# Performance work log

Hardware: AMD Instinct MI355X
Metric: run time of the kernel (lower is better)

The kernel has to match this reference:

```python
import jax, jax.numpy as jnp
import numpy as np

K_HEADS = 8
D_HEAD = 64
D = K_HEADS * D_HEAD  # 512
B, TP, TQ, N = 8, 48, 48, 256


def setup_inputs() -> dict:
    key = jax.random.key(0)
    ks = jax.random.split(key, 13)
    s = 1.0 / np.sqrt(D)
    inp = {
        "X": jax.random.normal(ks[0], (B, TP, N, D), jnp.float32),
        "STE_P": jax.random.normal(ks[1], (B, TP, N, D), jnp.float32),
        "STE_Q": jax.random.normal(ks[2], (B, TQ, N, D), jnp.float32),
        "Wq": jax.random.uniform(ks[3], (D, D), jnp.float32, -s, s),
        "bq": jax.random.uniform(ks[4], (D,), jnp.float32, -s, s),
        "Wk": jax.random.uniform(ks[5], (D, D), jnp.float32, -s, s),
        "bk": jax.random.uniform(ks[6], (D,), jnp.float32, -s, s),
        "Wv": jax.random.uniform(ks[7], (D, D), jnp.float32, -s, s),
        "bv": jax.random.uniform(ks[8], (D,), jnp.float32, -s, s),
        "W1": jax.random.uniform(ks[9], (D, D), jnp.float32, -s, s),
        "b1": jax.random.uniform(ks[10], (D,), jnp.float32, -s, s),
        "W2": jax.random.uniform(ks[11], (D, D), jnp.float32, -s, s),
        "b2": jax.random.uniform(ks[12], (D,), jnp.float32, -s, s),
    }
    return inp


def reference(X, STE_P, STE_Q, Wq, bq, Wk, bk, Wv, bv, W1, b1, W2, b2):
    # ReLU-fused QKV projections
    q = jax.nn.relu(STE_Q @ Wq + bq)  # [B, Tq, N, D]
    k = jax.nn.relu(STE_P @ Wk + bk)  # [B, Tp, N, D]
    v = jax.nn.relu(X @ Wv + bv)      # [B, Tp, N, D]

    # split(last, d) + cat(dim 0) == introduce head axis h of size K
    b, tq, n, _ = q.shape
    tp = k.shape[1]
    q = q.reshape(b, tq, n, K_HEADS, D_HEAD)
    k = k.reshape(b, tp, n, K_HEADS, D_HEAD)
    v = v.reshape(b, tp, n, K_HEADS, D_HEAD)

    # attention over the TIME axis, per node and head: scores [b,h,n,tq,tp]
    scale = 1.0 / jnp.sqrt(jnp.asarray(D_HEAD, q.dtype))
    attn = jnp.einsum('bqnhd,bpnhd->bhnqp', q, k) * scale
    attn = jax.nn.softmax(attn, axis=-1)
    out = jnp.einsum('bhnqp,bpnhd->bqnhd', attn, v).reshape(b, tq, n, D)

    out = jax.nn.relu(out @ W1 + b1) @ W2 + b2
    return out
```

## Files before the change

### kernel.cpp

```cpp
#include <hip/hip_runtime.h>

typedef _Float16 f16;
typedef __fp16 hf2 __attribute__((ext_vector_type(2)));
typedef _Float16 f16x4 __attribute__((ext_vector_type(4)));
typedef _Float16 f16x8 __attribute__((ext_vector_type(8)));
typedef float f32x4 __attribute__((ext_vector_type(4)));

typedef const __attribute__((address_space(1))) unsigned int guint;
typedef __attribute__((address_space(3))) unsigned int luint;
__device__ __forceinline__ void gl_lds16(const void* g, void* l) {
    __builtin_amdgcn_global_load_lds((guint*)g, (luint*)l, 16, 0, 0);
}
template <int N>
__device__ __forceinline__ void vmwait() {
    if constexpr (N == 8)       asm volatile("s_waitcnt vmcnt(8)" ::: "memory");
    else if constexpr (N == 6)  asm volatile("s_waitcnt vmcnt(6)" ::: "memory");
    else if constexpr (N == 4)  asm volatile("s_waitcnt vmcnt(4)" ::: "memory");
    else                        asm volatile("s_waitcnt vmcnt(0)" ::: "memory");
}
__device__ __forceinline__ void barrier_raw() { __builtin_amdgcn_s_barrier(); __builtin_amdgcn_sched_barrier(0); }
__device__ __forceinline__ void lgkm0() { asm volatile("s_waitcnt lgkmcnt(0)" ::: "memory"); }

__device__ __forceinline__ f16x8 pack8(float4 x0, float4 x1) {
    hf2 p0 = __builtin_amdgcn_cvt_pkrtz(x0.x, x0.y);
    hf2 p1 = __builtin_amdgcn_cvt_pkrtz(x0.z, x0.w);
    hf2 p2 = __builtin_amdgcn_cvt_pkrtz(x1.x, x1.y);
    hf2 p3 = __builtin_amdgcn_cvt_pkrtz(x1.z, x1.w);
    f16x8 h;
    h[0] = (f16)p0[0]; h[1] = (f16)p0[1]; h[2] = (f16)p1[0]; h[3] = (f16)p1[1];
    h[4] = (f16)p2[0]; h[5] = (f16)p2[1]; h[6] = (f16)p3[0]; h[7] = (f16)p3[1];
    return h;
}

__global__ __launch_bounds__(256) void wconv(const float* w0, const float* w1, const float* w2,
                                             const float* w3, const float* w4, f16* dst) {
    const float* src;
    switch (blockIdx.z) { case 0: src = w0; break; case 1: src = w1; break;
                          case 2: src = w2; break; case 3: src = w3; break; default: src = w4; }
    __shared__ float tile[32][33];
    int k0 = blockIdx.x * 32, n0 = blockIdx.y * 32;
    int t = threadIdx.x;
    int r = t >> 3, c4 = (t & 7) * 4;
    float4 v = *(const float4*)(src + (k0 + r) * 512 + n0 + c4);
    tile[r][c4 + 0] = v.x; tile[r][c4 + 1] = v.y; tile[r][c4 + 2] = v.z; tile[r][c4 + 3] = v.w;
    __syncthreads();
    f16x4 o;
    o[0] = (f16)tile[c4 + 0][r]; o[1] = (f16)tile[c4 + 1][r];
    o[2] = (f16)tile[c4 + 2][r]; o[3] = (f16)tile[c4 + 3][r];
    *(f16x4*)(dst + (size_t)blockIdx.z * 262144 + (n0 + r) * 512 + k0 + c4) = o;
}

__global__ __launch_bounds__(512, 2) void gemm_qkv3(const float* __restrict__ A0, const float* __restrict__ A1,
                                                    const float* __restrict__ A2,
                                                    const f16* __restrict__ B0, const f16* __restrict__ B1,
                                                    const f16* __restrict__ B2,
                                                    const float* __restrict__ bias0, const float* __restrict__ bias1,
                                                    const float* __restrict__ bias2,
                                                    f16* __restrict__ C0, f16* __restrict__ C1,
                                                    f16* __restrict__ C2) {
    constexpr int BUFSZ = 32768;
    __shared__ __align__(16) char smem[4 * BUFSZ];

    const int cpx = gridDim.x >> 3;
    const int orig = blockIdx.x;
    const int wgid = (orig & 7) * cpx + (orig >> 3);
    const int mid = wgid / 768;
    const int sub = wgid - mid * 768;
    const int by = sub & 1, bx = sub >> 1;
    const int r0 = bx * 256, c0 = by * 256;

    const float* A   = (mid == 0) ? A0 : (mid == 1) ? A1 : A2;
    const f16* Bt    = (mid == 0) ? B0 : (mid == 1) ? B1 : B2;
    const float* bias = (mid == 0) ? bias0 : (mid == 1) ? bias1 : bias2;
    f16* Cp          = (mid == 0) ? C0 : (mid == 1) ? C1 : C2;

    const int t = threadIdx.x, j = t & 63, w = t >> 6;
    const int lr = j & 15, lq = j >> 4;
    const int wr = (w >> 2) * 128, wc = (w & 3) * 64;

    const float* aS = A + (size_t)(r0 + (t >> 1)) * 512 + (t & 1) * 16;
    const int awRow = t >> 1;
    const int awS = (t >> 2) & 3;
    const int awc = (t & 1) * 2;
    const int aw0 = awRow * 64 + ((awc ^ awS) << 4);
    const int aw1 = awRow * 64 + (((awc + 1) ^ awS) << 4);

    const int srow = t >> 2;
    const int sblk = (t & 3) ^ ((t >> 3) & 3);
    const f16* bS = Bt + (size_t)(c0 + srow) * 512 + sblk * 8;
    const int dstT = t * 16;

    int aoff[8], boff[4];
#pragma unroll
    for (int m = 0; m < 8; m++) {
        int row = wr + m * 16 + lr;
        aoff[m] = row * 64 + ((lq ^ ((row >> 1) & 3)) << 4);
    }
#pragma unroll
    for (int nb = 0; nb < 4; nb++) {
        int row = wc + nb * 16 + lr;
        boff[nb] = 16384 + row * 64 + ((lq ^ ((row >> 1) & 3)) << 4);
    }

    f32x4 acc[8][4] = {};
    float4 rgA[4], rgB[4];

    auto loadTo = [&](int kt, float4* rg) {
        const float* p = aS + kt * 32;
        rg[0] = *(const float4*)p;
        rg[1] = *(const float4*)(p + 4);
        rg[2] = *(const float4*)(p + 8);
        rg[3] = *(const float4*)(p + 12);
    };
    auto writeA = [&](const float4* rg, int buf) {
        char* base = smem + buf * BUFSZ;
        *(f16x8*)(base + aw0) = pack8(rg[0], rg[1]);
        *(f16x8*)(base + aw1) = pack8(rg[2], rg[3]);
    };
    auto stageB = [&](int kt) {
        char* d = smem + (kt & 3) * BUFSZ + 16384 + dstT;
        const f16* s = bS + kt * 32;
        gl_lds16(s, d);
        gl_lds16(s + 65536, d + 8192);
    };

#define PHASE_A(kt, bfr)                                                    \
    do {                                                                    \
        const char* sb_ = smem + ((kt) & 3) * BUFSZ;                        \
        f16x8 afr[4];                                                       \
        _Pragma("unroll")                                                   \
        for (int nb = 0; nb < 4; nb++) bfr[nb] = *(const f16x8*)(sb_ + boff[nb]); \
        _Pragma("unroll")                                                   \
        for (int m = 0; m < 4; m++) afr[m] = *(const f16x8*)(sb_ + aoff[m]); \
        __builtin_amdgcn_s_setprio(1);                                      \
        _Pragma("unroll")                                                   \
        for (int m = 0; m < 4; m++)                                         \
            _Pragma("unroll")                                               \
            for (int nb = 0; nb < 4; nb++)                                  \
                acc[m][nb] = __builtin_amdgcn_mfma_f32_16x16x32_f16(afr[m], bfr[nb], acc[m][nb], 0, 0, 0); \
        __builtin_amdgcn_s_setprio(0);                                      \
    } while (0)

#define PHASE_B(kt, bfr)                                                    \
    do {                                                                    \
        const char* sb_ = smem + ((kt) & 3) * BUFSZ;                        \
        f16x8 afr2[4];                                                      \
        _Pragma("unroll")                                                   \
        for (int m = 0; m < 4; m++) afr2[m] = *(const f16x8*)(sb_ + aoff[m + 4]); \
        __builtin_amdgcn_s_setprio(1);                                      \
        _Pragma("unroll")                                                   \
        for (int m = 0; m < 4; m++)                                         \
            _Pragma("unroll")                                               \
            for (int nb = 0; nb < 4; nb++)                                  \
                acc[m + 4][nb] = __builtin_amdgcn_mfma_f32_16x16x32_f16(afr2[m], bfr[nb], acc[m + 4][nb], 0, 0, 0); \
        __builtin_amdgcn_s_setprio(0);                                      \
    } while (0)

    loadTo(0, rgA);
    stageB(0); stageB(1);
    loadTo(1, rgB);
    stageB(2);
    vmwait<8>();
    __builtin_amdgcn_sched_barrier(0);
    writeA(rgA, 0);
    lgkm0();
    barrier_raw();

#pragma unroll 1
    for (int k2 = 0; k2 < 8; ++k2) {
        {
            const int kt = 2 * k2;
            if (k2 <= 6) loadTo(kt + 2, rgA);
            if (k2 <= 6) vmwait<6>(); else vmwait<0>();
            __builtin_amdgcn_sched_barrier(0);
            writeA(rgB, (kt + 1) & 3);
            f16x8 bfr[4];
            PHASE_A(kt, bfr);
            barrier_raw();
            if (k2 <= 6) stageB(kt + 3);
            PHASE_B(kt, bfr);
            lgkm0();
            barrier_raw();
        }
        {
            const int kt = 2 * k2 + 1;
            if (k2 <= 6) loadTo(kt + 2, rgB);
            if (k2 <= 6) vmwait<6>(); else vmwait<0>();
            __builtin_amdgcn_sched_barrier(0);
            if (k2 <= 6) writeA(rgA, (kt + 1) & 3);
            f16x8 bfr[4];
            PHASE_A(kt, bfr);
            barrier_raw();
            if (k2 <= 5) stageB(kt + 3);
            PHASE_B(kt, bfr);
            lgkm0();
            barrier_raw();
        }
    }
#undef PHASE_A
#undef PHASE_B

#pragma unroll
    for (int nb = 0; nb < 4; nb++) {
        int col = wc + nb * 16 + lr;
        float b = bias[c0 + col];
#pragma unroll
        for (int m = 0; m < 8; m++) {
#pragma unroll
            for (int r = 0; r < 4; r++) {
                float v = fmaxf(acc[m][nb][r] + b, 0.0f);
                int row = wr + m * 16 + lq * 4 + r;
                int pblk = (col >> 3) ^ (row & 31);
                *(f16*)(smem + row * 512 + (pblk << 4) + (col & 7) * 2) = (f16)v;
            }
        }
    }
    lgkm0();
    barrier_raw();
#pragma unroll
    for (int i = 0; i < 16; i++) {
        int ci = i * 512 + t;
        int row = ci >> 5, blk = ci & 31;
        int pblk = blk ^ (row & 31);
        f16x8 vle = *(const f16x8*)(smem + row * 512 + (pblk << 4));
        *(f16x8*)(Cp + (size_t)(r0 + row) * 512 + c0 + blk * 8) = vle;
    }
}

template <bool RELU, bool O16>
__global__ __launch_bounds__(512, 2) void gemm_8ph(const f16* __restrict__ A,
                                                   const f16* __restrict__ Bt,
                                                   const float* __restrict__ bias,
                                                   void* __restrict__ Cp) {
    constexpr int BUFSZ = 32768;
    __shared__ __align__(16) char smem[4 * BUFSZ];

    const int cpx = gridDim.x >> 3;
    const int orig = blockIdx.x;
    const int wgid = (orig & 7) * cpx + (orig >> 3);
    const int by = wgid & 1;
    const int bx = wgid >> 1;
    const int r0 = bx * 256, c0 = by * 256;

    const int t = threadIdx.x;
    const int j = t & 63, w = t >> 6;
    const int lr = j & 15, lq = j >> 4;
    const int wr = (w >> 2) * 128, wc = (w & 3) * 64;

    const int srow = t >> 2;
    const int sblk = (t & 3) ^ ((t >> 3) & 3);
    const f16* aS = A  + (size_t)(r0 + srow) * 512 + sblk * 8;
    const f16* bS = Bt + (size_t)(c0 + srow) * 512 + sblk * 8;
    const int dstT = t * 16;

    int aoff[8], boff[4];
#pragma unroll
    for (int m = 0; m < 8; m++) {
        int row = wr + m * 16 + lr;
        aoff[m] = row * 64 + ((lq ^ ((row >> 1) & 3)) << 4);
    }
#pragma unroll
    for (int nb = 0; nb < 4; nb++) {
        int row = wc + nb * 16 + lr;
        boff[nb] = 16384 + row * 64 + ((lq ^ ((row >> 1) & 3)) << 4);
    }

    f32x4 acc[8][4] = {};

    auto stageA = [&](int kt) {
        char* d = smem + (kt & 3) * BUFSZ + dstT;
        const f16* s = aS + kt * 32;
        gl_lds16(s, d);
        gl_lds16(s + 65536, d + 8192);
    };
    auto stageB = [&](int kt) {
        char* d = smem + (kt & 3) * BUFSZ + 16384 + dstT;
        const f16* s = bS + kt * 32;
        gl_lds16(s, d);
        gl_lds16(s + 65536, d + 8192);
    };

    stageA(0); stageB(0); stageA(1); stageB(1); stageA(2); stageB(2);

#pragma unroll 1
    for (int kt = 0; kt < 16; ++kt) {
        const char* sb = smem + (kt & 3) * BUFSZ;
        if (kt <= 13)      vmwait<8>();
        else if (kt == 14) vmwait<4>();
        else               vmwait<0>();
        barrier_raw();
        if (kt < 13) stageA(kt + 3);
        f16x8 bfr[4], afr[4];
#pragma unroll
        for (int nb = 0; nb < 4; nb++) bfr[nb] = *(const f16x8*)(sb + boff[nb]);
#pragma unroll
        for (int m = 0; m < 4; m++) afr[m] = *(const f16x8*)(sb + aoff[m]);
        __builtin_amdgcn_s_setprio(1);
#pragma unroll
        for (int m = 0; m < 4; m++)
#pragma unroll
            for (int nb = 0; nb < 4; nb++)
                acc[m][nb] = __builtin_amdgcn_mfma_f32_16x16x32_f16(afr[m], bfr[nb], acc[m][nb], 0, 0, 0);
        __builtin_amdgcn_s_setprio(0);
        barrier_raw();
        if (kt < 13) stageB(kt + 3);
        f16x8 afr2[4];
#pragma unroll
        for (int m = 0; m < 4; m++) afr2[m] = *(const f16x8*)(sb + aoff[m + 4]);
        __builtin_amdgcn_s_setprio(1);
#pragma unroll
        for (int m = 0; m < 4; m++)
#pragma unroll
            for (int nb = 0; nb < 4; nb++)
                acc[m + 4][nb] = __builtin_amdgcn_mfma_f32_16x16x32_f16(afr2[m], bfr[nb], acc[m + 4][nb], 0, 0, 0);
        __builtin_amdgcn_s_setprio(0);
    }

    if (O16) {
#pragma unroll
        for (int nb = 0; nb < 4; nb++) {
            int col = wc + nb * 16 + lr;
            float b = bias[c0 + col];
#pragma unroll
            for (int m = 0; m < 8; m++) {
#pragma unroll
                for (int r = 0; r < 4; r++) {
                    float v = acc[m][nb][r] + b;
                    if (RELU) v = fmaxf(v, 0.0f);
                    int row = wr + m * 16 + lq * 4 + r;
                    int pblk = (col >> 3) ^ (row & 31);
                    *(f16*)(smem + row * 512 + (pblk << 4) + (col & 7) * 2) = (f16)v;
                }
            }
        }
        lgkm0();
        barrier_raw();
#pragma unroll
        for (int i = 0; i < 16; i++) {
            int ci = i * 512 + t;
            int row = ci >> 5, blk = ci & 31;
            int pblk = blk ^ (row & 31);
            f16x8 vle = *(const f16x8*)(smem + row * 512 + (pblk << 4));
            *(f16x8*)((f16*)Cp + (size_t)(r0 + row) * 512 + c0 + blk * 8) = vle;
        }
    } else {
#pragma unroll
        for (int nb = 0; nb < 4; nb++) {
            int col = c0 + wc + nb * 16 + lr;
            float b = bias[col];
#pragma unroll
            for (int m = 0; m < 8; m++) {
#pragma unroll
                for (int r = 0; r < 4; r++) {
                    float v = acc[m][nb][r] + b;
                    if (RELU) v = fmaxf(v, 0.0f);
                    size_t row = (size_t)(r0 + wr + m * 16 + lq * 4 + r);
                    ((float*)Cp)[row * 512 + col] = v;
                }
            }
        }
    }
}

__global__ __launch_bounds__(64) void attn_kernel(const f16* __restrict__ q,
                                                  const f16* __restrict__ k,
                                                  const f16* __restrict__ v,
                                                  f16* __restrict__ out) {
    const int h = blockIdx.x, n = blockIdx.y, b = blockIdx.z;
    __shared__ f16 sQ[48 * 72];
    __shared__ f16 sK[48 * 72];
    __shared__ f16 sP[48 * 72];
    __shared__ f16 sVt[64 * 72];
    const int l = threadIdx.x, lr = l & 15, lq = l >> 4;
    const size_t rowstride = 256 * 512;
    const size_t base = ((size_t)(b * 48) * 256 + n) * 512 + h * 64;

    const int pr = l >> 3, pc = (l & 7) * 8;
#pragma unroll
    for (int pass = 0; pass < 6; pass++) {
        int row = pass * 8 + pr;
        size_t g = base + (size_t)row * rowstride + pc;
        f16x8 qv = *(const f16x8*)(q + g);
        f16x8 kv = *(const f16x8*)(k + g);
        f16x8 vv = *(const f16x8*)(v + g);
        *(f16x8*)&sQ[row * 72 + pc] = qv;
        *(f16x8*)&sK[row * 72 + pc] = kv;
#pragma unroll
        for (int jj = 0; jj < 8; jj++) sVt[(pc + jj) * 72 + row] = vv[jj];
    }
    {
        f16x8 z = {};
        *(f16x8*)&sVt[l * 72 + 48] = z;
        *(f16x8*)&sVt[l * 72 + 56] = z;
        if (l < 48) { *(f16x8*)&sP[l * 72 + 48] = z; *(f16x8*)&sP[l * 72 + 56] = z; }
    }
    __syncthreads();

    f32x4 s[3][3] = {};
#pragma unroll
    for (int ks = 0; ks < 2; ks++) {
        f16x8 aq[3], bk[3];
#pragma unroll
        for (int m = 0; m < 3; m++)  aq[m] = *(const f16x8*)&sQ[(m * 16 + lr) * 72 + ks * 32 + lq * 8];
#pragma unroll
        for (int nb = 0; nb < 3; nb++) bk[nb] = *(const f16x8*)&sK[(nb * 16 + lr) * 72 + ks * 32 + lq * 8];
#pragma unroll
        for (int m = 0; m < 3; m++)
#pragma unroll
            for (int nb = 0; nb < 3; nb++)
                s[m][nb] = __builtin_amdgcn_mfma_f32_16x16x32_f16(aq[m], bk[nb], s[m][nb], 0, 0, 0);
    }

#pragma unroll
    for (int m = 0; m < 3; m++) {
#pragma unroll
        for (int r = 0; r < 4; r++) {
            float a0 = s[m][0][r] * 0.125f, a1 = s[m][1][r] * 0.125f, a2 = s[m][2][r] * 0.125f;
            float mx = fmaxf(a0, fmaxf(a1, a2));
#pragma unroll
            for (int d = 1; d < 16; d <<= 1) mx = fmaxf(mx, __shfl_xor(mx, d));
            float e0 = __expf(a0 - mx), e1 = __expf(a1 - mx), e2 = __expf(a2 - mx);
            float sm = e0 + e1 + e2;
#pragma unroll
            for (int d = 1; d < 16; d <<= 1) sm += __shfl_xor(sm, d);
            float inv = 1.0f / sm;
            int row = m * 16 + lq * 4 + r;
            sP[row * 72 + 0  + lr] = (f16)(e0 * inv);
            sP[row * 72 + 16 + lr] = (f16)(e1 * inv);
            sP[row * 72 + 32 + lr] = (f16)(e2 * inv);
        }
    }
    __syncthreads();

    f32x4 o[3][4] = {};
#pragma unroll
    for (int ks = 0; ks < 2; ks++) {
        f16x8 ap[3], bvv[4];
#pragma unroll
        for (int m = 0; m < 3; m++)  ap[m] = *(const f16x8*)&sP[(m * 16 + lr) * 72 + ks * 32 + lq * 8];
#pragma unroll
        for (int nb = 0; nb < 4; nb++) bvv[nb] = *(const f16x8*)&sVt[(nb * 16 + lr) * 72 + ks * 32 + lq * 8];
#pragma unroll
        for (int m = 0; m < 3; m++)
#pragma unroll
            for (int nb = 0; nb < 4; nb++)
                o[m][nb] = __builtin_amdgcn_mfma_f32_16x16x32_f16(ap[m], bvv[nb], o[m][nb], 0, 0, 0);
    }

    {
        char* so = (char*)sQ;
#pragma unroll
        for (int m = 0; m < 3; m++)
#pragma unroll
            for (int nb = 0; nb < 4; nb++)
#pragma unroll
                for (int r = 0; r < 4; r++) {
                    int row = m * 16 + lq * 4 + r;
                    int col = nb * 16 + lr;
                    int pblk = (col >> 3) ^ (row & 7);
                    *(f16*)(so + row * 128 + (pblk << 4) + (col & 7) * 2) = (f16)o[m][nb][r];
                }
        __syncthreads();
#pragma unroll
        for (int i = 0; i < 6; i++) {
            int ci = i * 64 + l;
            int row = ci >> 3, blk = ci & 7;
            int pblk = blk ^ (row & 7);
            f16x8 vle = *(const f16x8*)(so + row * 128 + (pblk << 4));
            *(f16x8*)(out + base + (size_t)row * rowstride + blk * 8) = vle;
        }
    }
}

extern "C" void kernel_launch(void* const* d_in, const int* in_sizes, int n_in,
                              void* d_out, int out_size, void* d_ws, size_t ws_size,
                              hipStream_t stream) {
    const float* X    = (const float*)d_in[0];
    const float* STEP = (const float*)d_in[1];
    const float* STEQ = (const float*)d_in[2];
    const float* Wq   = (const float*)d_in[3];
    const float* bq   = (const float*)d_in[4];
    const float* Wk   = (const float*)d_in[5];
    const float* bk   = (const float*)d_in[6];
    const float* Wv   = (const float*)d_in[7];
    const float* bv   = (const float*)d_in[8];
    const float* W1   = (const float*)d_in[9];
    const float* b1   = (const float*)d_in[10];
    const float* W2   = (const float*)d_in[11];
    const float* b2   = (const float*)d_in[12];
    float* out = (float*)d_out;

    const size_t MROWS = 98304;
    const size_t MBUF  = MROWS * 512;
    f16* ws  = (f16*)d_ws;
    f16* Wqt = ws;
    f16* Wkt = ws + 262144;
    f16* Wvt = ws + 524288;
    f16* W1t = ws + 786432;
    f16* W2t = ws + 1048576;
    f16* qb  = ws + 1310720;
    f16* kb  = qb + MBUF;
    f16* vb  = kb + MBUF;
    f16* hb  = kb;

    wconv<<<dim3(16, 16, 5), 256, 0, stream>>>(Wq, Wk, Wv, W1, W2, ws);

    gemm_qkv3<<<2304, 512, 0, stream>>>(STEQ, STEP, X, Wqt, Wkt, Wvt, bq, bk, bv, qb, kb, vb);

    attn_kernel<<<dim3(8, 256, 8), 64, 0, stream>>>(qb, kb, vb, qb);

    gemm_8ph<true,  true ><<<768, 512, 0, stream>>>(qb, W1t, b1, hb);
    gemm_8ph<false, false><<<768, 512, 0, stream>>>(hb, W2t, b2, out);
}
```

Before: 569.8 us.

## Double K-tile depth in QKV GEMM with two 64KB buffers and one barrier

Restructures the fused QKV projection GEMM main loop to use a 64-wide K tile with two 64KB LDS buffers instead of four 32KB buffers with 32-wide K. That halves the iteration count and drops one barrier per step, with an 8-way XOR swizzle for the wider rows. The 128KB of LDS forces occupancy down to one block per CU (launch bounds 512,1). It also doubles the per-thread register staging for A prefetch, so latency hiding now depends on intra-block pipelining rather than a second resident block.

```diff
diff --git a/kernel.cpp b/kernel.cpp
--- a/kernel.cpp
+++ b/kernel.cpp
@@ -50,7 +50,7 @@
     *(f16x4*)(dst + (size_t)blockIdx.z * 262144 + (n0 + r) * 512 + k0 + c4) = o;
 }
 
-__global__ __launch_bounds__(512, 2) void gemm_qkv3(const float* __restrict__ A0, const float* __restrict__ A1,
+__global__ __launch_bounds__(512, 1) void gemm_qkv3(const float* __restrict__ A0, const float* __restrict__ A1,
                                                     const float* __restrict__ A2,
                                                     const f16* __restrict__ B0, const f16* __restrict__ B1,
                                                     const f16* __restrict__ B2,
@@ -58,8 +58,9 @@
                                                     const float* __restrict__ bias2,
                                                     f16* __restrict__ C0, f16* __restrict__ C1,
                                                     f16* __restrict__ C2) {
-    constexpr int BUFSZ = 32768;
-    __shared__ __align__(16) char smem[4 * BUFSZ];
+    constexpr int ASZ = 32768;
+    constexpr int BUFSZ = 65536;
+    __shared__ __align__(16) char smem[2 * BUFSZ];
 
     const int cpx = gridDim.x >> 3;
     const int orig = blockIdx.x;
@@ -69,136 +70,114 @@
     const int by = sub & 1, bx = sub >> 1;
     const int r0 = bx * 256, c0 = by * 256;
 
-    const float* A   = (mid == 0) ? A0 : (mid == 1) ? A1 : A2;
-    const f16* Bt    = (mid == 0) ? B0 : (mid == 1) ? B1 : B2;
+    const float* A    = (mid == 0) ? A0 : (mid == 1) ? A1 : A2;
+    const f16* Bt     = (mid == 0) ? B0 : (mid == 1) ? B1 : B2;
     const float* bias = (mid == 0) ? bias0 : (mid == 1) ? bias1 : bias2;
-    f16* Cp          = (mid == 0) ? C0 : (mid == 1) ? C1 : C2;
+    f16* Cp           = (mid == 0) ? C0 : (mid == 1) ? C1 : C2;
 
     const int t = threadIdx.x, j = t & 63, w = t >> 6;
     const int lr = j & 15, lq = j >> 4;
     const int wr = (w >> 2) * 128, wc = (w & 3) * 64;
 
-    const float* aS = A + (size_t)(r0 + (t >> 1)) * 512 + (t & 1) * 16;
+    const float* aS = A + (size_t)(r0 + (t >> 1)) * 512 + (t & 1) * 32;
     const int awRow = t >> 1;
-    const int awS = (t >> 2) & 3;
-    const int awc = (t & 1) * 2;
-    const int aw0 = awRow * 64 + ((awc ^ awS) << 4);
-    const int aw1 = awRow * 64 + (((awc + 1) ^ awS) << 4);
-
-    const int srow = t >> 2;
-    const int sblk = (t & 3) ^ ((t >> 3) & 3);
-    const f16* bS = Bt + (size_t)(c0 + srow) * 512 + sblk * 8;
+    const int awS7 = awRow & 7;
+
+    const f16* bS = Bt + (size_t)(c0 + (t >> 3)) * 512 + ((t & 7) ^ ((t >> 3) & 7)) * 8;
     const int dstT = t * 16;
 
     int aoff[8], boff[4];
 #pragma unroll
     for (int m = 0; m < 8; m++) {
         int row = wr + m * 16 + lr;
-        aoff[m] = row * 64 + ((lq ^ ((row >> 1) & 3)) << 4);
+        aoff[m] = row * 128 + ((lq ^ (row & 7)) << 4);
     }
 #pragma unroll
     for (int nb = 0; nb < 4; nb++) {
         int row = wc + nb * 16 + lr;
-        boff[nb] = 16384 + row * 64 + ((lq ^ ((row >> 1) & 3)) << 4);
+        boff[nb] = row * 128 + ((lq ^ (row & 7)) << 4);
     }
 
     f32x4 acc[8][4] = {};
-    float4 rgA[4], rgB[4];
+    float4 rg0[8], rg1[8];
 
     auto loadTo = [&](int kt, float4* rg) {
-        const float* p = aS + kt * 32;
-        rg[0] = *(const float4*)p;
-        rg[1] = *(const float4*)(p + 4);
-        rg[2] = *(const float4*)(p + 8);
-        rg[3] = *(const float4*)(p + 12);
+        const float* p = aS + kt * 64;
+#pragma unroll
+        for (int i = 0; i < 8; i++) rg[i] = *(const float4*)(p + 4 * i);
     };
     auto writeA = [&](const float4* rg, int buf) {
-        char* base = smem + buf * BUFSZ;
-        *(f16x8*)(base + aw0) = pack8(rg[0], rg[1]);
-        *(f16x8*)(base + aw1) = pack8(rg[2], rg[3]);
-    };
-    auto stageB = [&](int kt) {
-        char* d = smem + (kt & 3) * BUFSZ + 16384 + dstT;
-        const f16* s = bS + kt * 32;
-        gl_lds16(s, d);
-        gl_lds16(s + 65536, d + 8192);
-    };
-
-#define PHASE_A(kt, bfr)                                                    \
-    do {                                                                    \
-        const char* sb_ = smem + ((kt) & 3) * BUFSZ;                        \
-        f16x8 afr[4];                                                       \
-        _Pragma("unroll")                                                   \
-        for (int nb = 0; nb < 4; nb++) bfr[nb] = *(const f16x8*)(sb_ + boff[nb]); \
-        _Pragma("unroll")                                                   \
-        for (int m = 0; m < 4; m++) afr[m] = *(const f16x8*)(sb_ + aoff[m]); \
-        __builtin_amdgcn_s_setprio(1);                                      \
-        _Pragma("unroll")                                                   \
-        for (int m = 0; m < 4; m++)                                         \
-            _Pragma("unroll")                                               \
-            for (int nb = 0; nb < 4; nb++)                                  \
-                acc[m][nb] = __builtin_amdgcn_mfma_f32_16x16x32_f16(afr[m], bfr[nb], acc[m][nb], 0, 0, 0); \
-        __builtin_amdgcn_s_setprio(0);                                      \
-    } while (0)
-
-#define PHASE_B(kt, bfr)                                                    \
-    do {                                                                    \
-        const char* sb_ = smem + ((kt) & 3) * BUFSZ;                        \
-        f16x8 afr2[4];                                                      \
-        _Pragma("unroll")                                                   \
-        for (int m = 0; m < 4; m++) afr2[m] = *(const f16x8*)(sb_ + aoff[m + 4]); \
-        __builtin_amdgcn_s_setprio(1);                                      \
-        _Pragma("unroll")                                                   \
-        for (int m = 0; m < 4; m++)                                         \
-            _Pragma("unroll")                                               \
-            for (int nb = 0; nb < 4; nb++)                                  \
-                acc[m + 4][nb] = __builtin_amdgcn_mfma_f32_16x16x32_f16(afr2[m], bfr[nb], acc[m + 4][nb], 0, 0, 0); \
-        __builtin_amdgcn_s_setprio(0);                                      \
-    } while (0)
-
-    loadTo(0, rgA);
-    stageB(0); stageB(1);
-    loadTo(1, rgB);
-    stageB(2);
+        char* base = smem + buf * BUFSZ + awRow * 128;
+#pragma unroll
+        for (int c = 0; c < 4; c++) {
+            int pblk = (((t & 1) * 4) + c) ^ awS7;
+            *(f16x8*)(base + pblk * 16) = pack8(rg[2 * c], rg[2 * c + 1]);
+        }
+    };
+    auto stageB = [&](int kt, int buf) {
+        char* d = smem + buf * BUFSZ + ASZ + dstT;
+        const f16* s = bS + kt * 64;
+#pragma unroll
+        for (int i = 0; i < 4; i++) gl_lds16(s + (size_t)i * 64 * 512, d + i * 8192);
+    };
+    auto compute = [&](int kt) {
+        const char* sb = smem + (kt & 1) * BUFSZ;
+#pragma unroll
+        for (int ks = 0; ks < 2; ks++) {
+            const int kx = ks * 64;
+            f16x8 bfr[4];
+#pragma unroll
+            for (int nb = 0; nb < 4; nb++) bfr[nb] = *(const f16x8*)(sb + ASZ + (boff[nb] ^ kx));
+#pragma unroll
+            for (int mh = 0; mh < 2; mh++) {
+                f16x8 afr[4];
+#pragma unroll
+                for (int m4 = 0; m4 < 4; m4++) afr[m4] = *(const f16x8*)(sb + (aoff[mh * 4 + m4] ^ kx));
+                __builtin_amdgcn_s_setprio(1);
+#pragma unroll
+                for (int m4 = 0; m4 < 4; m4++)
+#pragma unroll
+                    for (int nb = 0; nb < 4; nb++)
+                        acc[mh * 4 + m4][nb] = __builtin_amdgcn_mfma_f32_16x16x32_f16(afr[m4], bfr[nb], acc[mh * 4 + m4][nb], 0, 0, 0);
+                __builtin_amdgcn_s_setprio(0);
+            }
+        }
+    };
+
+    loadTo(0, rg0);
+    stageB(0, 0);
+    loadTo(1, rg1);
     vmwait<8>();
     __builtin_amdgcn_sched_barrier(0);
-    writeA(rgA, 0);
+    writeA(rg0, 0);
     lgkm0();
     barrier_raw();
 
 #pragma unroll 1
-    for (int k2 = 0; k2 < 8; ++k2) {
+    for (int k2 = 0; k2 < 4; ++k2) {
         {
             const int kt = 2 * k2;
-            if (k2 <= 6) loadTo(kt + 2, rgA);
-            if (k2 <= 6) vmwait<6>(); else vmwait<0>();
+            if (kt < 6) loadTo(kt + 2, rg0);
+            if (kt < 6) vmwait<8>(); else vmwait<0>();
             __builtin_amdgcn_sched_barrier(0);
-            writeA(rgB, (kt + 1) & 3);
-            f16x8 bfr[4];
-            PHASE_A(kt, bfr);
             barrier_raw();
-            if (k2 <= 6) stageB(kt + 3);
-            PHASE_B(kt, bfr);
+            stageB(kt + 1, (kt + 1) & 1);
+            writeA(rg1, (kt + 1) & 1);
+            compute(kt);
             lgkm0();
-            barrier_raw();
         }
         {
             const int kt = 2 * k2 + 1;
-            if (k2 <= 6) loadTo(kt + 2, rgB);
-            if (k2 <= 6) vmwait<6>(); else vmwait<0>();
+            if (kt < 6) loadTo(kt + 2, rg1);
+            if (kt < 6) vmwait<8>(); else vmwait<0>();
             __builtin_amdgcn_sched_barrier(0);
-            if (k2 <= 6) writeA(rgA, (kt + 1) & 3);
-            f16x8 bfr[4];
-            PHASE_A(kt, bfr);
             barrier_raw();
-            if (k2 <= 5) stageB(kt + 3);
-            PHASE_B(kt, bfr);
+            if (kt < 7) { stageB(kt + 1, (kt + 1) & 1); writeA(rg0, (kt + 1) & 1); }
+            compute(kt);
             lgkm0();
-            barrier_raw();
-        }
-    }
-#undef PHASE_A
-#undef PHASE_B
+        }
+    }
+    barrier_raw();
 
 #pragma unroll
     for (int nb = 0; nb < 4; nb++) {
```

Result: slower. 937.1 us (+64.5%).
